# Kernel optimization log

Hardware: AMD Instinct MI355X
Metric: run time of the kernel (lower is better)

The kernel has to match this reference:

```python
import jax, jax.numpy as jnp
import numpy as np

K_NEIGHBORS = 16  # module's k; KNN uses k+1 (includes self)


def setup_inputs() -> dict:
    key = jax.random.key(0)
    point_cloud = jax.random.normal(key, (2, 64, 8192), dtype=jnp.float32)
    return {"point_cloud": point_cloud}


def reference(point_cloud):
    # point_cloud: [B, D, N] -> [B, N, D]
    pc = jnp.transpose(point_cloud, (0, 2, 1))
    K = K_NEIGHBORS + 1

    # squared pairwise distances [B, N, N] (pytorch3d knn_points uses squared L2)
    sq = jnp.sum(pc * pc, axis=-1)  # [B, N]
    d2 = sq[:, :, None] + sq[:, None, :] - 2.0 * jnp.einsum('bnd,bmd->bnm', pc, pc)

    # K nearest (ascending distance; self first) via top_k on negative distances
    _, idx = jax.lax.top_k(-d2, K)  # idx: [B, N, K]

    # gather neighbors: [B, N, K, D]
    neighbors = jax.vmap(lambda p, i: p[i])(pc, idx)

    # neighbors -> [B, D, K, N]; central -> [B, D, K, N] (broadcast over K)
    neighbors = jnp.transpose(neighbors, (0, 3, 2, 1))
    central = jnp.broadcast_to(
        jnp.transpose(pc, (0, 2, 1))[:, :, None, :], neighbors.shape
    )

    edge_feature = jnp.concatenate([central, neighbors - central], axis=1)  # [B, 2D, K, N]
    idx_out = jnp.transpose(idx, (0, 2, 1))  # [B, K, N]
    return edge_feature, idx_out
```

## Files before the change

### kernel.cpp

```cpp
#include <hip/hip_runtime.h>

#define NPTS 8192
#define DIM 64
#define BATCH 2
#define KOUT 17
#define QCAP 40
#define THRANK 21
#define THSLACK 0.25f

typedef float f32x4 __attribute__((ext_vector_type(4)));
typedef short short8 __attribute__((ext_vector_type(8)));
typedef unsigned int uint4v __attribute__((ext_vector_type(4)));

#define MFMA16(A, B, C) __builtin_amdgcn_mfma_f32_16x16x32_bf16(A, B, C, 0, 0, 0)

__device__ __forceinline__ void gload16(const void* g, void* lds) {
  __builtin_amdgcn_global_load_lds((const __attribute__((address_space(1))) void*)g,
                                   (__attribute__((address_space(3))) void*)lds, 16, 0, 0);
}

__global__ __launch_bounds__(256)
void prep_kernel(const float* __restrict__ pc, ushort* __restrict__ phl,
                 float* __restrict__ pct, float* __restrict__ sq) {
  __shared__ double psum[256];
  int t = threadIdx.x;
  int u = t >> 5;
  int p = t & 31;
  int i = blockIdx.x * 32 + p;
  int b = i >> 13, n = i & (NPTS - 1);
  const float* g = pc + (size_t)b * DIM * NPTS + n;

  float x[8];
  short8 hv;
  double s = 0.0;
  #pragma unroll
  for (int e = 0; e < 8; ++e) {
    x[e] = g[(size_t)(u * 8 + e) * NPTS];
    s += (double)x[e] * (double)x[e];
    unsigned uu = __float_as_uint(x[e]);
    unsigned r = uu + (0x7fffu + ((uu >> 16) & 1));
    hv[e] = (short)((r >> 16) & 0xffffu);
  }
  int slot = u ^ (n & 7);
  *(short8*)(phl + (size_t)i * 64 + slot * 8) = hv;
  f32x4 v0 = {x[0], x[1], x[2], x[3]}, v1 = {x[4], x[5], x[6], x[7]};
  *(f32x4*)(pct + (size_t)i * 64 + u * 8) = v0;
  *(f32x4*)(pct + (size_t)i * 64 + u * 8 + 4) = v1;

  psum[u * 32 + p] = s;
  __syncthreads();
  if (t < 32) {
    double acc = 0.0;
    #pragma unroll
    for (int uu = 0; uu < 8; ++uu) acc += psum[uu * 32 + t];
    sq[blockIdx.x * 32 + t] = (float)(0.5 * acc);
  }
}

__global__ __launch_bounds__(256, 4)
void knn_kernel(const ushort* __restrict__ phl, const float* __restrict__ sq,
                ushort* __restrict__ cand) {
  __shared__ ushort Bt[4][64 * 64];
  __shared__ float TH[32];
  __shared__ int CNT[32];
  __shared__ ushort QU[32][QCAP];

  int t = threadIdx.x;
  int lane = t & 63;
  int w = t >> 6;
  int orig = blockIdx.x;
  int x8 = orig & 7;
  int b = x8 >> 2;
  int seg = (x8 >> 1) & 1;
  int row0 = ((orig >> 3) * 2 + (x8 & 1)) * 32;
  const ushort* pb = phl + (size_t)b * NPTS * 64;
  const float* sqb = sq + b * NPTS;

  int c15 = lane & 15, l4 = lane >> 4;
  int sw8 = c15 & 7;
  int so0 = (l4 ^ sw8) * 8;
  int so1 = ((4 + l4) ^ sw8) * 8;
  int colbase = seg * 4096;
  int lp = w * 16 + c15;
  const float* sqp = sqb + colbase + lp;

  short8 a[2][2];
  #pragma unroll
  for (int rg = 0; rg < 2; ++rg) {
    int n = row0 + rg * 16 + c15;
    const ushort* pr = pb + (size_t)n * 64;
    #pragma unroll
    for (int kk = 0; kk < 2; ++kk) {
      int slot = (kk * 4 + l4) ^ (n & 7);
      short8 v = *(const short8*)(pr + slot * 8);
      uint4v uv = *(uint4v*)&v;
      uv ^= 0x80008000u;
      a[kk][rg] = *(short8*)&uv;
    }
  }

#define STAGE(BUF, TILE) do { \
    const ushort* src_ = pb + (size_t)(colbase + (TILE) * 64 + w * 16 + (lane >> 3)) * 64 + (lane & 7) * 8; \
    ushort* dst_ = &Bt[BUF][w * 16 * 64]; \
    gload16(src_, dst_); \
    gload16(src_ + 512, dst_ + 512); \
  } while (0)

#define COMPKEYS(BUF, SQV, C0, C1) \
    const ushort* bt_ = &Bt[BUF][lp * 64]; \
    short8 b0 = *(const short8*)(bt_ + so0); \
    short8 b1 = *(const short8*)(bt_ + so1); \
    f32x4 C0 = {SQV, SQV, SQV, SQV}, C1 = C0; \
    C0 = MFMA16(a[0][0], b0, C0); C1 = MFMA16(a[0][1], b0, C1); \
    C0 = MFMA16(a[1][0], b1, C0); C1 = MFMA16(a[1][1], b1, C1);

#define VMW9 asm volatile("s_waitcnt vmcnt(9)" ::: "memory")

  float k1[2][4], k2[2][4];
  #pragma unroll
  for (int rg = 0; rg < 2; ++rg)
    #pragma unroll
    for (int r = 0; r < 4; ++r) { k1[rg][r] = __builtin_inff(); k2[rg][r] = __builtin_inff(); }

#define SELA(C0, C1) { \
    _Pragma("unroll") \
    for (int r = 0; r < 4; ++r) { \
      k2[0][r] = __builtin_amdgcn_fmed3f(C0[r], k1[0][r], k2[0][r]); \
      k1[0][r] = fminf(C0[r], k1[0][r]); \
      k2[1][r] = __builtin_amdgcn_fmed3f(C1[r], k1[1][r], k2[1][r]); \
      k1[1][r] = fminf(C1[r], k1[1][r]); \
    } }

  {
    asm volatile("s_waitcnt vmcnt(0)" ::: "memory");
    STAGE(0, 0); float sqA = sqp[0];
    STAGE(1, 1); float sqB = sqp[64];
    STAGE(2, 2); float sqC = sqp[128];
    float sqD;
    for (int g = 0; g < 16; ++g) {
      int t4 = g * 4;
      STAGE(3, (t4 + 3) & 63); sqD = sqp[((t4 + 3) & 63) * 64];
      VMW9; { COMPKEYS(0, sqA, c0, c1); SELA(c0, c1); }
      STAGE(0, (t4 + 4) & 63); sqA = sqp[((t4 + 4) & 63) * 64];
      VMW9; { COMPKEYS(1, sqB, c0, c1); SELA(c0, c1); }
      STAGE(1, (t4 + 5) & 63); sqB = sqp[((t4 + 5) & 63) * 64];
      VMW9; { COMPKEYS(2, sqC, c0, c1); SELA(c0, c1); }
      STAGE(2, (t4 + 6) & 63); sqC = sqp[((t4 + 6) & 63) * 64];
      VMW9; { COMPKEYS(3, sqD, c0, c1); SELA(c0, c1); }
    }
  }

  __syncthreads();
  float* KT = (float*)&Bt[0][0];
  float* KT2 = (float*)&Bt[2][0];
  #pragma unroll
  for (int rg = 0; rg < 2; ++rg)
    #pragma unroll
    for (int r = 0; r < 4; ++r) {
      int row = rg * 16 + l4 * 4 + r;
      KT[row * 128 + (w * 16 + c15) * 2] = k1[rg][r];
      KT[row * 128 + (w * 16 + c15) * 2 + 1] = k2[rg][r];
    }
  __syncthreads();
  #pragma unroll
  for (int it = 0; it < 4; ++it) {
    int idx = t + it * 256;
    int row = idx >> 5, j = idx & 31;
    float a1 = KT[row * 128 + j * 2], a2 = KT[row * 128 + j * 2 + 1];
    float b1 = KT[row * 128 + 64 + j * 2], b2 = KT[row * 128 + 64 + j * 2 + 1];
    KT2[row * 64 + j * 2] = fminf(a1, b1);
    KT2[row * 64 + j * 2 + 1] = fminf(fmaxf(a1, b1), fminf(a2, b2));
  }
  __syncthreads();

  {
    int row = t >> 3;
    int j0 = (t & 7) * 8;
    const f32x4* vr4 = (const f32x4*)(KT2 + row * 64);
    float vj[8];
    *(f32x4*)vj = vr4[(t & 7) * 2];
    *(f32x4*)(vj + 4) = vr4[(t & 7) * 2 + 1];
    int rank[8];
    #pragma unroll
    for (int jj = 0; jj < 8; ++jj) rank[jj] = 0;
    for (int m4 = 0; m4 < 16; ++m4) {
      f32x4 vm = vr4[m4];
      #pragma unroll
      for (int e = 0; e < 4; ++e) {
        int m = m4 * 4 + e;
        float ve = vm[e];
        #pragma unroll
        for (int jj = 0; jj < 8; ++jj)
          rank[jj] += (ve < vj[jj] || (ve == vj[jj] && m < j0 + jj)) ? 1 : 0;
      }
    }
    #pragma unroll
    for (int jj = 0; jj < 8; ++jj)
      if (rank[jj] == THRANK) TH[row] = vj[jj];
    if (t < 32) CNT[t] = 0;
  }
  __syncthreads();
  float th0[4], th1[4];
  #pragma unroll
  for (int r = 0; r < 4; ++r) {
    th0[r] = TH[l4 * 4 + r] + THSLACK;
    th1[r] = TH[16 + l4 * 4 + r] + THSLACK;
  }

#define SELB(C0, C1, GCOL) { \
    _Pragma("unroll") \
    for (int r = 0; r < 4; ++r) { \
      if (C0[r] <= th0[r]) { \
        int rw = l4 * 4 + r; \
        int pos = atomicAdd(&CNT[rw], 1); \
        if (pos < QCAP) QU[rw][pos] = (ushort)(GCOL); \
      } \
      if (C1[r] <= th1[r]) { \
        int rw = 16 + l4 * 4 + r; \
        int pos = atomicAdd(&CNT[rw], 1); \
        if (pos < QCAP) QU[rw][pos] = (ushort)(GCOL); \
      } \
    } }

  {
    asm volatile("s_waitcnt vmcnt(0)" ::: "memory");
    STAGE(0, 0); float sqA = sqp[0];
    STAGE(1, 1); float sqB = sqp[64];
    STAGE(2, 2); float sqC = sqp[128];
    float sqD;
    for (int g = 0; g < 16; ++g) {
      int t4 = g * 4;
      int gc = colbase + t4 * 64 + lp;
      STAGE(3, (t4 + 3) & 63); sqD = sqp[((t4 + 3) & 63) * 64];
      VMW9; { COMPKEYS(0, sqA, c0, c1); SELB(c0, c1, gc); }
      STAGE(0, (t4 + 4) & 63); sqA = sqp[((t4 + 4) & 63) * 64];
      VMW9; { COMPKEYS(1, sqB, c0, c1); SELB(c0, c1, gc + 64); }
      STAGE(1, (t4 + 5) & 63); sqB = sqp[((t4 + 5) & 63) * 64];
      VMW9; { COMPKEYS(2, sqC, c0, c1); SELB(c0, c1, gc + 128); }
      STAGE(2, (t4 + 6) & 63); sqC = sqp[((t4 + 6) & 63) * 64];
      VMW9; { COMPKEYS(3, sqD, c0, c1); SELB(c0, c1, gc + 192); }
    }
  }

  __syncthreads();
  for (int i = t; i < 32 * QCAP; i += 256) {
    int row = i / QCAP, s2 = i % QCAP;
    int c2 = CNT[row]; if (c2 > QCAP) c2 = QCAP;
    ushort v = (s2 < c2) ? QU[row][s2] : (ushort)0xFFFFu;
    cand[((size_t)(b * NPTS + row0 + row) * 2 + seg) * QCAP + s2] = v;
  }
}

__global__ void refine_kernel(const float* __restrict__ pct, const ushort* __restrict__ cand,
                              int* __restrict__ knn, float* __restrict__ idxf) {
  int gw = (blockIdx.x * 256 + threadIdx.x) >> 6;
  int lane = threadIdx.x & 63;
  int b = gw >> 13, n = gw & (NPTS - 1);
  const float* pcb = pct + (size_t)b * NPTS * 64;
  const ushort* cb = cand + (size_t)gw * (2 * QCAP);
  const float* qp = pcb + (size_t)n * 64;

  unsigned ciA = cb[lane];
  unsigned ciB = (lane < 2 * QCAP - 64) ? (unsigned)cb[64 + lane] : 0xFFFFu;
  double dA = __builtin_inf(), dB = __builtin_inf();
  if (ciA != 0xFFFFu) {
    const float* cp = pcb + (size_t)ciA * 64;
    double s = 0.0;
    #pragma unroll
    for (int u = 0; u < 16; ++u) {
      f32x4 cv = *(const f32x4*)(cp + u * 4);
      f32x4 qv = *(const f32x4*)(qp + u * 4);
      #pragma unroll
      for (int e = 0; e < 4; ++e) {
        double diff = (double)cv[e] - (double)qv[e];
        s = fma(diff, diff, s);
      }
    }
    dA = s;
  }
  if (ciB != 0xFFFFu) {
    const float* cp = pcb + (size_t)ciB * 64;
    double s = 0.0;
    #pragma unroll
    for (int u = 0; u < 16; ++u) {
      f32x4 cv = *(const f32x4*)(cp + u * 4);
      f32x4 qv = *(const f32x4*)(qp + u * 4);
      #pragma unroll
      for (int e = 0; e < 4; ++e) {
        double diff = (double)cv[e] - (double)qv[e];
        s = fma(diff, diff, s);
      }
    }
    dB = s;
  }

  int rA = 0, rB = 0;
  for (int j = 0; j < 64; ++j) {
    double dk = __shfl(dA, j);
    unsigned ik = (unsigned)__shfl((int)ciA, j);
    rA += ((dk < dA) || (dk == dA && ik < ciA)) ? 1 : 0;
    rB += ((dk < dB) || (dk == dB && ik < ciB)) ? 1 : 0;
  }
  for (int j = 0; j < 2 * QCAP - 64; ++j) {
    double dk = __shfl(dB, j);
    unsigned ik = (unsigned)__shfl((int)ciB, j);
    rA += ((dk < dA) || (dk == dA && ik < ciA)) ? 1 : 0;
    rB += ((dk < dB) || (dk == dB && ik < ciB)) ? 1 : 0;
  }
  if (ciA != 0xFFFFu && rA < KOUT) {
    size_t o = ((size_t)b * KOUT + rA) * NPTS + n;
    knn[o] = (int)ciA;
    idxf[o] = (float)ciA;
  }
  if (lane < 2 * QCAP - 64 && ciB != 0xFFFFu && rB < KOUT) {
    size_t o = ((size_t)b * KOUT + rB) * NPTS + n;
    knn[o] = (int)ciB;
    idxf[o] = (float)ciB;
  }
}

__global__ __launch_bounds__(256)
void edge_kernel(const float* __restrict__ pc, const int* __restrict__ knn,
                 float* __restrict__ out) {
  int n = (blockIdx.x * 256 + threadIdx.x) * 4;
  int z = blockIdx.y;
  int b = z >> 6, c = z & 63;
  const float* row = pc + ((size_t)b * DIM + c) * NPTS;
  f32x4 central = *(const f32x4*)(row + n);
  size_t base = (((size_t)b * 2 * DIM + c) * KOUT) * NPTS + n;
  const int* kb = knn + (size_t)b * KOUT * NPTS + n;
  #pragma unroll
  for (int k = 0; k < KOUT; ++k) {
    int4 nb = *(const int4*)(kb + (size_t)k * NPTS);
    f32x4 nv = {row[nb.x], row[nb.y], row[nb.z], row[nb.w]};
    *(f32x4*)(out + base + (size_t)k * NPTS) = central;
    *(f32x4*)(out + base + (size_t)(DIM * KOUT + k) * NPTS) = nv - central;
  }
}

extern "C" void kernel_launch(void* const* d_in, const int* in_sizes, int n_in,
                              void* d_out, int out_size, void* d_ws, size_t ws_size,
                              hipStream_t stream) {
  const float* pc = (const float*)d_in[0];
  float* out = (float*)d_out;
  char* ws = (char*)d_ws;
  ushort* phl = (ushort*)ws;
  float* pct  = (float*)(ws + (size_t)2 * 1024 * 1024);
  float* sq   = (float*)(ws + (size_t)6 * 1024 * 1024);
  ushort* cand = (ushort*)(ws + (size_t)6 * 1024 * 1024 + 65536);
  int* knn    = (int*)(ws + (size_t)6 * 1024 * 1024 + 65536 + (size_t)16384 * 2 * QCAP * 2);

  float* idxf = out + (size_t)BATCH * 2 * DIM * KOUT * NPTS;

  prep_kernel<<<512, 256, 0, stream>>>(pc, phl, pct, sq);
  knn_kernel<<<1024, 256, 0, stream>>>(phl, sq, cand);
  refine_kernel<<<4096, 256, 0, stream>>>(pct, cand, knn, idxf);
  edge_kernel<<<dim3(NPTS / 1024, BATCH * DIM), 256, 0, stream>>>(pc, knn, out);
}
```

Before: 197.3 us.

## Widen KNN column tiles to 128 with double buffering instead of 4-deep ring

Each wave now processes 32 columns per tile (two 16-column MFMA groups) using 128-column tiles, double-buffered, in place of four 64-column buffers. Each tile issues four async LDS loads per lane, and the wait count changes to vmcnt(6). Per-lane top-2 state is doubled and merged before the shared-memory reduction. The aim is more MFMA work per wait and fewer loop iterations and waits, at the cost of a shallower prefetch pipeline and more registers, which may lower occupancy.

```diff
diff --git a/kernel.cpp b/kernel.cpp
--- a/kernel.cpp
+++ b/kernel.cpp
@@ -60,7 +60,7 @@
 __global__ __launch_bounds__(256, 4)
 void knn_kernel(const ushort* __restrict__ phl, const float* __restrict__ sq,
                 ushort* __restrict__ cand) {
-  __shared__ ushort Bt[4][64 * 64];
+  __shared__ ushort Bt[2][128 * 64];
   __shared__ float TH[32];
   __shared__ int CNT[32];
   __shared__ ushort QU[32][QCAP];
@@ -81,8 +81,8 @@
   int so0 = (l4 ^ sw8) * 8;
   int so1 = ((4 + l4) ^ sw8) * 8;
   int colbase = seg * 4096;
-  int lp = w * 16 + c15;
-  const float* sqp = sqb + colbase + lp;
+  const float* sqp0 = sqb + colbase + w * 32 + c15;
+  const float* sqp1 = sqp0 + 16;
 
   short8 a[2][2];
   #pragma unroll
@@ -100,66 +100,82 @@
   }
 
 #define STAGE(BUF, TILE) do { \
-    const ushort* src_ = pb + (size_t)(colbase + (TILE) * 64 + w * 16 + (lane >> 3)) * 64 + (lane & 7) * 8; \
-    ushort* dst_ = &Bt[BUF][w * 16 * 64]; \
-    gload16(src_, dst_); \
-    gload16(src_ + 512, dst_ + 512); \
+    const ushort* src_ = pb + (size_t)(colbase + (TILE) * 128 + w * 32 + (lane >> 3)) * 64 + (lane & 7) * 8; \
+    ushort* dst_ = &Bt[BUF][w * 32 * 64]; \
+    gload16(src_,         dst_); \
+    gload16(src_ + 512,   dst_ + 512); \
+    gload16(src_ + 1024,  dst_ + 1024); \
+    gload16(src_ + 1536,  dst_ + 1536); \
   } while (0)
 
-#define COMPKEYS(BUF, SQV, C0, C1) \
-    const ushort* bt_ = &Bt[BUF][lp * 64]; \
-    short8 b0 = *(const short8*)(bt_ + so0); \
-    short8 b1 = *(const short8*)(bt_ + so1); \
-    f32x4 C0 = {SQV, SQV, SQV, SQV}, C1 = C0; \
-    C0 = MFMA16(a[0][0], b0, C0); C1 = MFMA16(a[0][1], b0, C1); \
-    C0 = MFMA16(a[1][0], b1, C0); C1 = MFMA16(a[1][1], b1, C1);
-
-#define VMW9 asm volatile("s_waitcnt vmcnt(9)" ::: "memory")
-
-  float k1[2][4], k2[2][4];
+#define COMPALL(BUF, S0, S1) \
+    const ushort* btA_ = &Bt[BUF][(w * 32 + c15) * 64]; \
+    const ushort* btB_ = btA_ + 16 * 64; \
+    short8 p0_ = *(const short8*)(btA_ + so0); \
+    short8 p1_ = *(const short8*)(btA_ + so1); \
+    short8 q0_ = *(const short8*)(btB_ + so0); \
+    short8 q1_ = *(const short8*)(btB_ + so1); \
+    f32x4 cA0 = {S0, S0, S0, S0}, cA1 = cA0; \
+    f32x4 cB0 = {S1, S1, S1, S1}, cB1 = cB0; \
+    cA0 = MFMA16(a[0][0], p0_, cA0); cA1 = MFMA16(a[0][1], p0_, cA1); \
+    cB0 = MFMA16(a[0][0], q0_, cB0); cB1 = MFMA16(a[0][1], q0_, cB1); \
+    cA0 = MFMA16(a[1][0], p1_, cA0); cA1 = MFMA16(a[1][1], p1_, cA1); \
+    cB0 = MFMA16(a[1][0], q1_, cB0); cB1 = MFMA16(a[1][1], q1_, cB1);
+
+#define VMW6 asm volatile("s_waitcnt vmcnt(6)" ::: "memory")
+#define VMW0 asm volatile("s_waitcnt vmcnt(0)" ::: "memory")
+
+  float k1[2][2][4], k2[2][2][4];
   #pragma unroll
   for (int rg = 0; rg < 2; ++rg)
     #pragma unroll
-    for (int r = 0; r < 4; ++r) { k1[rg][r] = __builtin_inff(); k2[rg][r] = __builtin_inff(); }
-
-#define SELA(C0, C1) { \
+    for (int cg = 0; cg < 2; ++cg)
+      #pragma unroll
+      for (int r = 0; r < 4; ++r) { k1[rg][cg][r] = __builtin_inff(); k2[rg][cg][r] = __builtin_inff(); }
+
+#define SELA(BUF, S0, S1) { \
+    COMPALL(BUF, S0, S1); \
     _Pragma("unroll") \
     for (int r = 0; r < 4; ++r) { \
-      k2[0][r] = __builtin_amdgcn_fmed3f(C0[r], k1[0][r], k2[0][r]); \
-      k1[0][r] = fminf(C0[r], k1[0][r]); \
-      k2[1][r] = __builtin_amdgcn_fmed3f(C1[r], k1[1][r], k2[1][r]); \
-      k1[1][r] = fminf(C1[r], k1[1][r]); \
+      k2[0][0][r] = __builtin_amdgcn_fmed3f(cA0[r], k1[0][0][r], k2[0][0][r]); \
+      k1[0][0][r] = fminf(cA0[r], k1[0][0][r]); \
+      k2[1][0][r] = __builtin_amdgcn_fmed3f(cA1[r], k1[1][0][r], k2[1][0][r]); \
+      k1[1][0][r] = fminf(cA1[r], k1[1][0][r]); \
+      k2[0][1][r] = __builtin_amdgcn_fmed3f(cB0[r], k1[0][1][r], k2[0][1][r]); \
+      k1[0][1][r] = fminf(cB0[r], k1[0][1][r]); \
+      k2[1][1][r] = __builtin_amdgcn_fmed3f(cB1[r], k1[1][1][r], k2[1][1][r]); \
+      k1[1][1][r] = fminf(cB1[r], k1[1][1][r]); \
     } }
 
   {
-    asm volatile("s_waitcnt vmcnt(0)" ::: "memory");
-    STAGE(0, 0); float sqA = sqp[0];
-    STAGE(1, 1); float sqB = sqp[64];
-    STAGE(2, 2); float sqC = sqp[128];
-    float sqD;
-    for (int g = 0; g < 16; ++g) {
-      int t4 = g * 4;
-      STAGE(3, (t4 + 3) & 63); sqD = sqp[((t4 + 3) & 63) * 64];
-      VMW9; { COMPKEYS(0, sqA, c0, c1); SELA(c0, c1); }
-      STAGE(0, (t4 + 4) & 63); sqA = sqp[((t4 + 4) & 63) * 64];
-      VMW9; { COMPKEYS(1, sqB, c0, c1); SELA(c0, c1); }
-      STAGE(1, (t4 + 5) & 63); sqB = sqp[((t4 + 5) & 63) * 64];
-      VMW9; { COMPKEYS(2, sqC, c0, c1); SELA(c0, c1); }
-      STAGE(2, (t4 + 6) & 63); sqC = sqp[((t4 + 6) & 63) * 64];
-      VMW9; { COMPKEYS(3, sqD, c0, c1); SELA(c0, c1); }
-    }
+    VMW0;
+    STAGE(0, 0); float s0A = sqp0[0], s1A = sqp1[0];
+    float s0B, s1B;
+    for (int tt = 0; tt < 30; tt += 2) {
+      STAGE(1, tt + 1); s0B = sqp0[(tt + 1) * 128]; s1B = sqp1[(tt + 1) * 128];
+      VMW6; { SELA(0, s0A, s1A); }
+      STAGE(0, tt + 2); s0A = sqp0[(tt + 2) * 128]; s1A = sqp1[(tt + 2) * 128];
+      VMW6; { SELA(1, s0B, s1B); }
+    }
+    STAGE(1, 31); s0B = sqp0[31 * 128]; s1B = sqp1[31 * 128];
+    VMW6; { SELA(0, s0A, s1A); }
+    VMW0; { SELA(1, s0B, s1B); }
   }
 
   __syncthreads();
   float* KT = (float*)&Bt[0][0];
-  float* KT2 = (float*)&Bt[2][0];
+  float* KT2 = (float*)&Bt[1][0];
   #pragma unroll
   for (int rg = 0; rg < 2; ++rg)
     #pragma unroll
     for (int r = 0; r < 4; ++r) {
+      float x1 = k1[rg][0][r], x2 = k2[rg][0][r];
+      float y1 = k1[rg][1][r], y2 = k2[rg][1][r];
+      float m1 = fminf(x1, y1);
+      float m2 = fminf(fmaxf(x1, y1), fminf(x2, y2));
       int row = rg * 16 + l4 * 4 + r;
-      KT[row * 128 + (w * 16 + c15) * 2] = k1[rg][r];
-      KT[row * 128 + (w * 16 + c15) * 2 + 1] = k2[rg][r];
+      KT[row * 128 + (w * 16 + c15) * 2] = m1;
+      KT[row * 128 + (w * 16 + c15) * 2 + 1] = m2;
     }
   __syncthreads();
   #pragma unroll
@@ -207,39 +223,48 @@
     th1[r] = TH[16 + l4 * 4 + r] + THSLACK;
   }
 
-#define SELB(C0, C1, GCOL) { \
+#define SELB(BUF, S0, S1, GC0) { \
+    COMPALL(BUF, S0, S1); \
+    int gc1_ = (GC0) + 16; \
     _Pragma("unroll") \
     for (int r = 0; r < 4; ++r) { \
-      if (C0[r] <= th0[r]) { \
+      if (cA0[r] <= th0[r]) { \
         int rw = l4 * 4 + r; \
         int pos = atomicAdd(&CNT[rw], 1); \
-        if (pos < QCAP) QU[rw][pos] = (ushort)(GCOL); \
+        if (pos < QCAP) QU[rw][pos] = (ushort)(GC0); \
       } \
-      if (C1[r] <= th1[r]) { \
+      if (cA1[r] <= th1[r]) { \
         int rw = 16 + l4 * 4 + r; \
         int pos = atomicAdd(&CNT[rw], 1); \
-        if (pos < QCAP) QU[rw][pos] = (ushort)(GCOL); \
+        if (pos < QCAP) QU[rw][pos] = (ushort)(GC0); \
+      } \
+      if (cB0[r] <= th0[r]) { \
+        int rw = l4 * 4 + r; \
+        int pos = atomicAdd(&CNT[rw], 1); \
+        if (pos < QCAP) QU[rw][pos] = (ushort)gc1_; \
+      } \
+      if (cB1[r] <= th1[r]) { \
+        int rw = 16 + l4 * 4 + r; \
+        int pos = atomicAdd(&CNT[rw], 1); \
+        if (pos < QCAP) QU[rw][pos] = (ushort)gc1_; \
       } \
     } }
 
   {
-    asm volatile("s_waitcnt vmcnt(0)" ::: "memory");
-    STAGE(0, 0); float sqA = sqp[0];
-    STAGE(1, 1); float sqB = sqp[64];
-    STAGE(2, 2); float sqC = sqp[128];
-    float sqD;
-    for (int g = 0; g < 16; ++g) {
-      int t4 = g * 4;
-      int gc = colbase + t4 * 64 + lp;
-      STAGE(3, (t4 + 3) & 63); sqD = sqp[((t4 + 3) & 63) * 64];
-      VMW9; { COMPKEYS(0, sqA, c0, c1); SELB(c0, c1, gc); }
-      STAGE(0, (t4 + 4) & 63); sqA = sqp[((t4 + 4) & 63) * 64];
-      VMW9; { COMPKEYS(1, sqB, c0, c1); SELB(c0, c1, gc + 64); }
-      STAGE(1, (t4 + 5) & 63); sqB = sqp[((t4 + 5) & 63) * 64];
-      VMW9; { COMPKEYS(2, sqC, c0, c1); SELB(c0, c1, gc + 128); }
-      STAGE(2, (t4 + 6) & 63); sqC = sqp[((t4 + 6) & 63) * 64];
-      VMW9; { COMPKEYS(3, sqD, c0, c1); SELB(c0, c1, gc + 192); }
-    }
+    VMW0;
+    STAGE(0, 0); float s0A = sqp0[0], s1A = sqp1[0];
+    float s0B, s1B;
+    int gcA = colbase + w * 32 + c15;
+    for (int tt = 0; tt < 30; tt += 2) {
+      STAGE(1, tt + 1); s0B = sqp0[(tt + 1) * 128]; s1B = sqp1[(tt + 1) * 128];
+      VMW6; { SELB(0, s0A, s1A, gcA); }
+      STAGE(0, tt + 2); s0A = sqp0[(tt + 2) * 128]; s1A = sqp1[(tt + 2) * 128];
+      VMW6; { SELB(1, s0B, s1B, gcA + 128); }
+      gcA += 256;
+    }
+    STAGE(1, 31); s0B = sqp0[31 * 128]; s1B = sqp1[31 * 128];
+    VMW6; { SELB(0, s0A, s1A, gcA); }
+    VMW0; { SELB(1, s0B, s1B, gcA + 128); }
   }
 
   __syncthreads();
```

Measured after the change: 191.7 us. 1.03x faster.
